# Kernel tuning notes

Hardware: AMD Instinct MI355X
Metric: run time of the kernel (lower is better)

Reference implementation:

```python
import jax, jax.numpy as jnp
import numpy as np

HID = 512      # hidden_size
IN = 1         # encoder/decoder input feature size
OUT = 1        # linear output size (feeds back as decoder input)
SEQ = 1000     # encoder sequence length
BATCH = 512
TGT = 1000     # target_len (decoder steps)


def setup_inputs() -> dict:
    key = jax.random.key(0)
    ks = jax.random.split(key, 11)
    s = 1.0 / np.sqrt(HID)  # PyTorch LSTM/Linear uniform init scale
    u = lambda k, shp: jax.random.uniform(k, shp, jnp.float32, -s, s)
    return {
        "input_batch": jax.random.normal(ks[0], (SEQ, BATCH, IN), jnp.float32),
        "enc_Wih": u(ks[1], (4 * HID, IN)),
        "enc_Whh": u(ks[2], (4 * HID, HID)),
        "enc_bih": u(ks[3], (4 * HID,)),
        "enc_bhh": u(ks[4], (4 * HID,)),
        "dec_Wih": u(ks[5], (4 * HID, OUT)),
        "dec_Whh": u(ks[6], (4 * HID, HID)),
        "dec_bih": u(ks[7], (4 * HID,)),
        "dec_bhh": u(ks[8], (4 * HID,)),
        "lin_W": u(ks[9], (OUT, HID)),
        "lin_b": u(ks[10], (OUT,)),
    }


def _lstm_cell(x, h, c, Wih, Whh, b):
    # PyTorch gate order: i, f, g, o
    gates = x @ Wih.T + h @ Whh.T + b  # [B, 4H]
    i, f, g, o = jnp.split(gates, 4, axis=-1)
    c = jax.nn.sigmoid(f) * c + jax.nn.sigmoid(i) * jnp.tanh(g)
    h = jax.nn.sigmoid(o) * jnp.tanh(c)
    return h, c


def reference(input_batch, enc_Wih, enc_Whh, enc_bih, enc_bhh,
              dec_Wih, dec_Whh, dec_bih, dec_bhh, lin_W, lin_b):
    batch = input_batch.shape[1]
    b_enc = enc_bih + enc_bhh
    b_dec = dec_bih + dec_bhh
    h0 = jnp.zeros((batch, HID), input_batch.dtype)

    # --- encoder: scan over SEQ time steps, zero initial state ---
    def enc_step(carry, x_t):
        h, c = carry
        h, c = _lstm_cell(x_t, h, c, enc_Wih, enc_Whh, b_enc)
        return (h, c), None

    (h, c), _ = jax.lax.scan(enc_step, (h0, h0), input_batch)

    x0 = jnp.zeros((batch, OUT), input_batch.dtype)

    def dec_step(carry, _):
        h, c, x = carry
        h, c = _lstm_cell(x, h, c, dec_Wih, dec_Whh, b_dec)
        pred = h @ lin_W.T + lin_b  # [B, OUT]
        return (h, c, pred), pred

    _, outputs = jax.lax.scan(dec_step, (h, c, x0), None, length=TGT)
    return outputs  # [TGT, BATCH, OUT]
```

## Files before the change

### kernel.cpp

```cpp
#include <hip/hip_runtime.h>


typedef _Float16 f16x8 __attribute__((ext_vector_type(8)));
typedef _Float16 f16x2 __attribute__((ext_vector_type(2)));
typedef float    f32x4 __attribute__((ext_vector_type(4)));
typedef unsigned long long u64;
typedef unsigned int u32;

#define GLOAD_LDS16(gp, lp)                                                    \
  __builtin_amdgcn_global_load_lds(                                            \
      (const __attribute__((address_space(1))) void*)(gp),                     \
      (__attribute__((address_space(3))) void*)(lp), 16, 0, 17)

__device__ __forceinline__ void store_h4_llc(_Float16* p, f16x2 v) {
  __hip_atomic_store((u32*)p, __builtin_bit_cast(u32, v),
                     __ATOMIC_RELAXED, __HIP_MEMORY_SCOPE_AGENT);
}

__device__ __forceinline__ float sigm(float x) {
  return __builtin_amdgcn_rcpf(1.0f + __expf(-x));
}
__device__ __forceinline__ float tanh_fast(float x) {
  float r = __expf(-2.0f*fabsf(x));
  float t = (1.0f - r)*__builtin_amdgcn_rcpf(1.0f + r);
  return copysignf(t, x);
}

__global__ void init_zero(float* __restrict__ out, int nout,
                          float* __restrict__ wsf, int nws) {
  int i = blockIdx.x*blockDim.x + threadIdx.x;
  int st = gridDim.x*blockDim.x;
  for (int j=i; j<nout; j+=st)
    __hip_atomic_store(&out[j], 0.f, __ATOMIC_RELAXED, __HIP_MEMORY_SCOPE_AGENT);
  for (int j=i; j<nws;  j+=st)
    __hip_atomic_store(&wsf[j], 0.f, __ATOMIC_RELAXED, __HIP_MEMORY_SCOPE_AGENT);
}

__global__ __launch_bounds__(256, 2) void lstm_main(
    const float* __restrict__ xin,
    const float* __restrict__ encWih, const float* __restrict__ encWhh,
    const float* __restrict__ enc_bih, const float* __restrict__ enc_bhh,
    const float* __restrict__ decWih, const float* __restrict__ decWhh,
    const float* __restrict__ dec_bih, const float* __restrict__ dec_bhh,
    const float* __restrict__ linW, const float* __restrict__ linb,
    float* __restrict__ out,
    _Float16* __restrict__ hbuf,
    int* __restrict__ flags)
{
  __shared__ f16x8 h_lds[2048];
  __shared__ float gates[32][68];

  const int bid = blockIdx.x, tid = threadIdx.x;
  const int rb = bid >> 5, hb = bid & 31;
  const int wid = tid >> 6, lane = tid & 63;
  const int lcol = lane & 15, lq = lane >> 4, kq = lq*8;

  const int b_local = tid >> 3, u0 = (tid & 7)*2;
  const int bg = rb*32 + b_local;
  const int jh0 = hb*16 + u0;

  float linw[2];
  #pragma unroll
  for (int u=0; u<2; ++u) linw[u] = linW[jh0+u];
  const float linbv = linb[0];

  f16x8 wHi[16], wLo[16];
  float biasv[8], wihv[8];
  float c[2] = {0.f, 0.f};
  int* myflag = flags + bid*32;
  const int* pollp = flags + (rb*32 + (lane & 31))*32;

  int goff[8];
  #pragma unroll
  for (int i=0; i<8; ++i) {
    const int cch = i*256 + tid;
    const int frag = cch >> 6;
    const int ks = frag >> 1, half = frag & 1;
    const int row_local = half*16 + (cch & 15);
    goff[i] = row_local*512 + ks*32 + ((cch >> 4) & 3)*8;
  }

  auto loadW = [&](const float* Whh, const float* bih, const float* bhh,
                   const float* Wih) {
    const int g = wid;
    const float* wr = Whh + (size_t)(g*512 + hb*16 + lcol)*512;
    #pragma unroll
    for (int ks=0; ks<16; ++ks) {
      f16x8 hi, lo;
      #pragma unroll
      for (int i=0; i<8; ++i) {
        float w = wr[ks*32 + kq + i];
        _Float16 hh = (_Float16)w;
        float hf = (float)hh;
        float rem = (w - hf)*2048.0f;
        if (fabsf(hf) < 6.104e-5f) { hh = (_Float16)0.0f; rem = w*2048.0f; }
        hi[i] = hh; lo[i] = (_Float16)rem;
      }
      wHi[ks] = hi; wLo[ks] = lo;
    }
    #pragma unroll
    for (int gg=0; gg<4; ++gg)
      #pragma unroll
      for (int u=0; u<2; ++u) {
        int j = gg*512 + jh0 + u;
        biasv[gg*2+u] = bih[j] + bhh[j];
        wihv[gg*2+u]  = Wih[j];
      }
  };

  loadW(encWhh, enc_bih, enc_bhh, encWih);

  for (int s=0; s<2000; ++s) {
    if (s == 1000) loadW(decWhh, dec_bih, dec_bhh, decWih);
    const bool dec = (s >= 1000);
    const int td = s - 1000;
    const _Float16* hr = hbuf + (size_t)((s+1)&1)*(512*512);
    _Float16*       hw = hbuf + (size_t)( s   &1)*(512*512);

    const _Float16* hrb = hr + (size_t)rb*32*512;
    f16x8* ldst = &h_lds[(size_t)wid*64];

    float x;
    if (!dec) x = xin[(size_t)s*512 + bg];
    else if (td == 0) x = 0.0f;
    else x = __hip_atomic_load(&out[(size_t)(td-1)*512 + bg],
                               __ATOMIC_RELAXED, __HIP_MEMORY_SCOPE_AGENT);

    #pragma unroll
    for (int i=0; i<8; ++i)
      GLOAD_LDS16(hrb + goff[i], ldst + i*256);
    __syncthreads();

    f32x4 accH[2], accL[2];
    accH[0] = {0.f,0.f,0.f,0.f}; accH[1] = {0.f,0.f,0.f,0.f};
    accL[0] = {0.f,0.f,0.f,0.f}; accL[1] = {0.f,0.f,0.f,0.f};

    #pragma unroll
    for (int ks=0; ks<16; ++ks) {
      const f16x8 a0 = h_lds[(ks*2+0)*64 + lane];
      const f16x8 a1 = h_lds[(ks*2+1)*64 + lane];
      accH[0] = __builtin_amdgcn_mfma_f32_16x16x32_f16(a0, wHi[ks], accH[0], 0,0,0);
      accH[1] = __builtin_amdgcn_mfma_f32_16x16x32_f16(a1, wHi[ks], accH[1], 0,0,0);
      accL[0] = __builtin_amdgcn_mfma_f32_16x16x32_f16(a0, wLo[ks], accL[0], 0,0,0);
      accL[1] = __builtin_amdgcn_mfma_f32_16x16x32_f16(a1, wLo[ks], accL[1], 0,0,0);
    }

    #pragma unroll
    for (int rt=0; rt<2; ++rt) {
      f32x4 v = accH[rt] + accL[rt]*(1.0f/2048.0f);
      const int col  = wid*16 + lcol;
      const int row0 = rt*16 + lq*4;
      #pragma unroll
      for (int i=0; i<4; ++i) gates[row0+i][col] = v[i];
    }
    __syncthreads();

    const float* grow = gates[b_local];
    f16x2 hv2;
    float sp = 0.f;
    #pragma unroll
    for (int u=0; u<2; ++u) {
      float ai = grow[ 0 + u0+u] + biasv[0+u] + x*wihv[0+u];
      float af = grow[16 + u0+u] + biasv[2+u] + x*wihv[2+u];
      float ag = grow[32 + u0+u] + biasv[4+u] + x*wihv[4+u];
      float ao = grow[48 + u0+u] + biasv[6+u] + x*wihv[6+u];
      float iv = sigm(ai);
      float fv = sigm(af);
      float gv = tanh_fast(ag);
      float ov = sigm(ao);
      float cn = fv*c[u] + iv*gv;
      c[u] = cn;
      float hv = ov*tanh_fast(cn);
      hv2[u] = (_Float16)hv;
      sp += hv*linw[u];
    }
    store_h4_llc(hw + (size_t)bg*512 + jh0, hv2);

    if (dec) {
      sp += __shfl_xor(sp, 1);
      sp += __shfl_xor(sp, 2);
      sp += __shfl_xor(sp, 4);
      if ((tid & 7) == 0) {
        float v = sp + (hb == 0 ? linbv : 0.f);
        __hip_atomic_fetch_add(&out[(size_t)td*512 + bg], v,
                               __ATOMIC_RELAXED, __HIP_MEMORY_SCOPE_AGENT);
      }
    }

    if (s != 1999) {
      asm volatile("s_waitcnt vmcnt(0)" ::: "memory");
      __syncthreads();
      const int av = s + 1;
      if (tid == 0)
        __hip_atomic_store(myflag, av, __ATOMIC_RELAXED, __HIP_MEMORY_SCOPE_AGENT);
      if (wid == 0) {
        while (!__all(__hip_atomic_load(pollp, __ATOMIC_RELAXED,
                                        __HIP_MEMORY_SCOPE_AGENT) >= av)) { }
      }
      __syncthreads();
    }
  }
}

extern "C" void kernel_launch(void* const* d_in, const int* in_sizes, int n_in,
                              void* d_out, int out_size, void* d_ws, size_t ws_size,
                              hipStream_t stream) {
  const float* xin     = (const float*)d_in[0];
  const float* encWih  = (const float*)d_in[1];
  const float* encWhh  = (const float*)d_in[2];
  const float* enc_bih = (const float*)d_in[3];
  const float* enc_bhh = (const float*)d_in[4];
  const float* decWih  = (const float*)d_in[5];
  const float* decWhh  = (const float*)d_in[6];
  const float* dec_bih = (const float*)d_in[7];
  const float* dec_bhh = (const float*)d_in[8];
  const float* linW    = (const float*)d_in[9];
  const float* linb    = (const float*)d_in[10];
  float* out = (float*)d_out;
  char* ws = (char*)d_ws;
  int* flags = (int*)ws;
  _Float16* hbuf = (_Float16*)(ws + 65536);

  init_zero<<<512, 256, 0, stream>>>(out, 1000*512, (float*)ws,
                                     (65536 + 2*512*512*2)/4);

  lstm_main<<<dim3(512), dim3(256), 0, stream>>>(
      xin, encWih, encWhh, enc_bih, enc_bhh,
      decWih, decWhh, dec_bih, dec_bhh,
      linW, linb, out, hbuf, flags);
}
```

Baseline: 12.53 ms.

## Split batch across twice as many blocks, 16 rows each

```diff
diff --git a/kernel.cpp b/kernel.cpp
--- a/kernel.cpp
+++ b/kernel.cpp
@@ -4,7 +4,6 @@
 typedef _Float16 f16x8 __attribute__((ext_vector_type(8)));
 typedef _Float16 f16x2 __attribute__((ext_vector_type(2)));
 typedef float    f32x4 __attribute__((ext_vector_type(4)));
-typedef unsigned long long u64;
 typedef unsigned int u32;
 
 #define GLOAD_LDS16(gp, lp)                                                    \
@@ -36,7 +35,7 @@
     __hip_atomic_store(&wsf[j], 0.f, __ATOMIC_RELAXED, __HIP_MEMORY_SCOPE_AGENT);
 }
 
-__global__ __launch_bounds__(256, 2) void lstm_main(
+__global__ __launch_bounds__(256, 4) void lstm_main(
     const float* __restrict__ xin,
     const float* __restrict__ encWih, const float* __restrict__ encWhh,
     const float* __restrict__ enc_bih, const float* __restrict__ enc_bhh,
@@ -47,16 +46,18 @@
     _Float16* __restrict__ hbuf,
     int* __restrict__ flags)
 {
-  __shared__ f16x8 h_lds[2048];
-  __shared__ float gates[32][68];
+  __shared__ f16x8 h_lds[1024];
+  __shared__ float gates[16][68];
 
   const int bid = blockIdx.x, tid = threadIdx.x;
   const int rb = bid >> 5, hb = bid & 31;
   const int wid = tid >> 6, lane = tid & 63;
   const int lcol = lane & 15, lq = lane >> 4, kq = lq*8;
 
-  const int b_local = tid >> 3, u0 = (tid & 7)*2;
-  const int bg = rb*32 + b_local;
+  const bool pw = (tid < 128);
+  const int b_local = tid >> 3;
+  const int u0 = (tid & 7)*2;
+  const int bg = rb*16 + (b_local & 15);
   const int jh0 = hb*16 + u0;
 
   float linw[2];
@@ -70,14 +71,12 @@
   int* myflag = flags + bid*32;
   const int* pollp = flags + (rb*32 + (lane & 31))*32;
 
-  int goff[8];
+  int goff[4];
   #pragma unroll
-  for (int i=0; i<8; ++i) {
+  for (int i=0; i<4; ++i) {
     const int cch = i*256 + tid;
-    const int frag = cch >> 6;
-    const int ks = frag >> 1, half = frag & 1;
-    const int row_local = half*16 + (cch & 15);
-    goff[i] = row_local*512 + ks*32 + ((cch >> 4) & 3)*8;
+    const int ks = cch >> 6, l = cch & 63;
+    goff[i] = (l & 15)*512 + ks*32 + (l >> 4)*8;
   }
 
   auto loadW = [&](const float* Whh, const float* bih, const float* bhh,
@@ -117,73 +116,70 @@
     const _Float16* hr = hbuf + (size_t)((s+1)&1)*(512*512);
     _Float16*       hw = hbuf + (size_t)( s   &1)*(512*512);
 
-    const _Float16* hrb = hr + (size_t)rb*32*512;
+    const _Float16* hrb = hr + (size_t)rb*16*512;
     f16x8* ldst = &h_lds[(size_t)wid*64];
 
-    float x;
-    if (!dec) x = xin[(size_t)s*512 + bg];
-    else if (td == 0) x = 0.0f;
-    else x = __hip_atomic_load(&out[(size_t)(td-1)*512 + bg],
-                               __ATOMIC_RELAXED, __HIP_MEMORY_SCOPE_AGENT);
-
-    #pragma unroll
-    for (int i=0; i<8; ++i)
+    float x = 0.0f;
+    if (pw) {
+      if (!dec) x = xin[(size_t)s*512 + bg];
+      else if (td > 0)
+        x = __hip_atomic_load(&out[(size_t)(td-1)*512 + bg],
+                              __ATOMIC_RELAXED, __HIP_MEMORY_SCOPE_AGENT);
+    }
+
+    #pragma unroll
+    for (int i=0; i<4; ++i)
       GLOAD_LDS16(hrb + goff[i], ldst + i*256);
     __syncthreads();
 
-    f32x4 accH[2], accL[2];
-    accH[0] = {0.f,0.f,0.f,0.f}; accH[1] = {0.f,0.f,0.f,0.f};
-    accL[0] = {0.f,0.f,0.f,0.f}; accL[1] = {0.f,0.f,0.f,0.f};
-
+    f32x4 accH = {0.f,0.f,0.f,0.f}, accL = {0.f,0.f,0.f,0.f};
     #pragma unroll
     for (int ks=0; ks<16; ++ks) {
-      const f16x8 a0 = h_lds[(ks*2+0)*64 + lane];
-      const f16x8 a1 = h_lds[(ks*2+1)*64 + lane];
-      accH[0] = __builtin_amdgcn_mfma_f32_16x16x32_f16(a0, wHi[ks], accH[0], 0,0,0);
-      accH[1] = __builtin_amdgcn_mfma_f32_16x16x32_f16(a1, wHi[ks], accH[1], 0,0,0);
-      accL[0] = __builtin_amdgcn_mfma_f32_16x16x32_f16(a0, wLo[ks], accL[0], 0,0,0);
-      accL[1] = __builtin_amdgcn_mfma_f32_16x16x32_f16(a1, wLo[ks], accL[1], 0,0,0);
-    }
-
-    #pragma unroll
-    for (int rt=0; rt<2; ++rt) {
-      f32x4 v = accH[rt] + accL[rt]*(1.0f/2048.0f);
+      const f16x8 a = h_lds[ks*64 + lane];
+      accH = __builtin_amdgcn_mfma_f32_16x16x32_f16(a, wHi[ks], accH, 0,0,0);
+      accL = __builtin_amdgcn_mfma_f32_16x16x32_f16(a, wLo[ks], accL, 0,0,0);
+    }
+
+    {
+      f32x4 v = accH + accL*(1.0f/2048.0f);
       const int col  = wid*16 + lcol;
-      const int row0 = rt*16 + lq*4;
+      const int row0 = lq*4;
       #pragma unroll
       for (int i=0; i<4; ++i) gates[row0+i][col] = v[i];
     }
     __syncthreads();
 
-    const float* grow = gates[b_local];
-    f16x2 hv2;
-    float sp = 0.f;
-    #pragma unroll
-    for (int u=0; u<2; ++u) {
-      float ai = grow[ 0 + u0+u] + biasv[0+u] + x*wihv[0+u];
-      float af = grow[16 + u0+u] + biasv[2+u] + x*wihv[2+u];
-      float ag = grow[32 + u0+u] + biasv[4+u] + x*wihv[4+u];
-      float ao = grow[48 + u0+u] + biasv[6+u] + x*wihv[6+u];
-      float iv = sigm(ai);
-      float fv = sigm(af);
-      float gv = tanh_fast(ag);
-      float ov = sigm(ao);
-      float cn = fv*c[u] + iv*gv;
-      c[u] = cn;
-      float hv = ov*tanh_fast(cn);
-      hv2[u] = (_Float16)hv;
-      sp += hv*linw[u];
-    }
-    store_h4_llc(hw + (size_t)bg*512 + jh0, hv2);
-
-    if (dec) {
-      sp += __shfl_xor(sp, 1);
-      sp += __shfl_xor(sp, 2);
-      sp += __shfl_xor(sp, 4);
-      if ((tid & 7) == 0) {
-        float v = sp + (hb == 0 ? linbv : 0.f);
-        __hip_atomic_fetch_add(&out[(size_t)td*512 + bg], v,
-                               __ATOMIC_RELAXED, __HIP_MEMORY_SCOPE_AGENT);
+    if (pw) {
+      const float* grow = gates[b_local & 15];
+      f16x2 hv2;
+      float sp = 0.f;
+      #pragma unroll
+      for (int u=0; u<2; ++u) {
+        float ai = grow[ 0 + u0+u] + biasv[0+u] + x*wihv[0+u];
+        float af = grow[16 + u0+u] + biasv[2+u] + x*wihv[2+u];
+        float ag = grow[32 + u0+u] + biasv[4+u] + x*wihv[4+u];
+        float ao = grow[48 + u0+u] + biasv[6+u] + x*wihv[6+u];
+        float iv = sigm(ai);
+        float fv = sigm(af);
+        float gv = tanh_fast(ag);
+        float ov = sigm(ao);
+        float cn = fv*c[u] + iv*gv;
+        c[u] = cn;
+        float hv = ov*tanh_fast(cn);
+        hv2[u] = (_Float16)hv;
+        sp += hv*linw[u];
+      }
+      store_h4_llc(hw + (size_t)bg*512 + jh0, hv2);
+
+      if (dec) {
+        sp += __shfl_xor(sp, 1);
+        sp += __shfl_xor(sp, 2);
+        sp += __shfl_xor(sp, 4);
+        if ((tid & 7) == 0) {
+          float v = sp + (hb == 0 ? linbv : 0.f);
+          __hip_atomic_fetch_add(&out[(size_t)td*512 + bg], v,
+                                 __ATOMIC_RELAXED, __HIP_MEMORY_SCOPE_AGENT);
+        }
       }
     }
 
@@ -219,12 +215,12 @@
   float* out = (float*)d_out;
   char* ws = (char*)d_ws;
   int* flags = (int*)ws;
-  _Float16* hbuf = (_Float16*)(ws + 65536);
+  _Float16* hbuf = (_Float16*)(ws + 131072);
 
   init_zero<<<512, 256, 0, stream>>>(out, 1000*512, (float*)ws,
-                                     (65536 + 2*512*512*2)/4);
-
-  lstm_main<<<dim3(512), dim3(256), 0, stream>>>(
+                                     (131072 + 2*512*512*2)/4);
+
+  lstm_main<<<dim3(1024), dim3(256), 0, stream>>>(
       xin, encWih, encWhh, enc_bih, enc_bhh,
       decWih, decWhh, dec_bih, dec_bhh,
       linW, linb, out, hbuf, flags);
```

New measurement: 25.43 ms. +102.9%, slower.

## Use per-wave flags and a partial-sum buffer to shorten the inter-block barrier

Applied to the files above, without the earlier changes.

```diff
diff --git a/kernel.cpp b/kernel.cpp
--- a/kernel.cpp
+++ b/kernel.cpp
@@ -4,6 +4,7 @@
 typedef _Float16 f16x8 __attribute__((ext_vector_type(8)));
 typedef _Float16 f16x2 __attribute__((ext_vector_type(2)));
 typedef float    f32x4 __attribute__((ext_vector_type(4)));
+typedef float    f32x2 __attribute__((ext_vector_type(2)));
 typedef unsigned long long u64;
 typedef unsigned int u32;
 
@@ -15,6 +16,11 @@
 __device__ __forceinline__ void store_h4_llc(_Float16* p, f16x2 v) {
   __hip_atomic_store((u32*)p, __builtin_bit_cast(u32, v),
                      __ATOMIC_RELAXED, __HIP_MEMORY_SCOPE_AGENT);
+}
+__device__ __forceinline__ f32x2 load_f2_llc(const float* p) {
+  u64 v = __hip_atomic_load((const u64*)p, __ATOMIC_RELAXED,
+                            __HIP_MEMORY_SCOPE_AGENT);
+  return __builtin_bit_cast(f32x2, v);
 }
 
 __device__ __forceinline__ float sigm(float x) {
@@ -45,7 +51,8 @@
     const float* __restrict__ linW, const float* __restrict__ linb,
     float* __restrict__ out,
     _Float16* __restrict__ hbuf,
-    int* __restrict__ flags)
+    int* __restrict__ flags,
+    float* __restrict__ part)
 {
   __shared__ f16x8 h_lds[2048];
   __shared__ float gates[32][68];
@@ -67,8 +74,9 @@
   f16x8 wHi[16], wLo[16];
   float biasv[8], wihv[8];
   float c[2] = {0.f, 0.f};
-  int* myflag = flags + bid*32;
-  const int* pollp = flags + (rb*32 + (lane & 31))*32;
+  int* myflag = flags + (bid*4 + wid)*32;
+  const int* p0 = flags + (rb*128 + lane)*32;
+  const int* p1 = flags + (rb*128 + 64 + lane)*32;
 
   int goff[8];
   #pragma unroll
@@ -120,11 +128,19 @@
     const _Float16* hrb = hr + (size_t)rb*32*512;
     f16x8* ldst = &h_lds[(size_t)wid*64];
 
-    float x;
-    if (!dec) x = xin[(size_t)s*512 + bg];
-    else if (td == 0) x = 0.0f;
-    else x = __hip_atomic_load(&out[(size_t)(td-1)*512 + bg],
-                               __ATOMIC_RELAXED, __HIP_MEMORY_SCOPE_AGENT);
+    float x = 0.0f;
+    if (!dec) {
+      x = xin[(size_t)s*512 + bg];
+    } else if (td > 0) {
+      const float* pb = part + (size_t)((td-1)&1)*16384 + bg*32 + (tid&7)*4;
+      f32x2 a = load_f2_llc(pb);
+      f32x2 b2 = load_f2_llc(pb + 2);
+      float sm = a[0] + a[1] + b2[0] + b2[1];
+      sm += __shfl_xor(sm, 1);
+      sm += __shfl_xor(sm, 2);
+      sm += __shfl_xor(sm, 4);
+      x = sm + linbv;
+    }
 
     #pragma unroll
     for (int i=0; i<8; ++i)
@@ -180,24 +196,36 @@
       sp += __shfl_xor(sp, 1);
       sp += __shfl_xor(sp, 2);
       sp += __shfl_xor(sp, 4);
-      if ((tid & 7) == 0) {
-        float v = sp + (hb == 0 ? linbv : 0.f);
-        __hip_atomic_fetch_add(&out[(size_t)td*512 + bg], v,
-                               __ATOMIC_RELAXED, __HIP_MEMORY_SCOPE_AGENT);
-      }
+      if ((tid & 7) == 0)
+        __hip_atomic_store(&part[(size_t)(td&1)*16384 + bg*32 + hb], sp,
+                           __ATOMIC_RELAXED, __HIP_MEMORY_SCOPE_AGENT);
     }
 
     if (s != 1999) {
       asm volatile("s_waitcnt vmcnt(0)" ::: "memory");
-      __syncthreads();
+      if (lane == 0)
+        __hip_atomic_store(myflag, s + 1, __ATOMIC_RELAXED,
+                           __HIP_MEMORY_SCOPE_AGENT);
+    }
+
+    if (dec && (tid & 7) == 0) {
+      float v = sp + (hb == 0 ? linbv : 0.f);
+      __hip_atomic_fetch_add(&out[(size_t)td*512 + bg], v,
+                             __ATOMIC_RELAXED, __HIP_MEMORY_SCOPE_AGENT);
+    }
+
+    if (s != 1999) {
       const int av = s + 1;
-      if (tid == 0)
-        __hip_atomic_store(myflag, av, __ATOMIC_RELAXED, __HIP_MEMORY_SCOPE_AGENT);
       if (wid == 0) {
-        while (!__all(__hip_atomic_load(pollp, __ATOMIC_RELAXED,
-                                        __HIP_MEMORY_SCOPE_AGENT) >= av)) { }
+        while (true) {
+          int f0 = __hip_atomic_load(p0, __ATOMIC_RELAXED, __HIP_MEMORY_SCOPE_AGENT);
+          int f1 = __hip_atomic_load(p1, __ATOMIC_RELAXED, __HIP_MEMORY_SCOPE_AGENT);
+          if (__all((f0 < av ? f0 : f1 < av ? f1 : av) >= av)) break;
+        }
       }
       __syncthreads();
+    } else {
+      asm volatile("s_waitcnt vmcnt(0)" ::: "memory");
     }
   }
 }
@@ -219,13 +247,14 @@
   float* out = (float*)d_out;
   char* ws = (char*)d_ws;
   int* flags = (int*)ws;
-  _Float16* hbuf = (_Float16*)(ws + 65536);
+  _Float16* hbuf = (_Float16*)(ws + 262144);
+  float* part = (float*)(ws + 262144 + 1048576);
 
   init_zero<<<512, 256, 0, stream>>>(out, 1000*512, (float*)ws,
-                                     (65536 + 2*512*512*2)/4);
+                                     (262144 + 1048576 + 131072)/4);
 
   lstm_main<<<dim3(512), dim3(256), 0, stream>>>(
       xin, encWih, encWhh, enc_bih, enc_bhh,
       decWih, decWhh, dec_bih, dec_bhh,
-      linW, linb, out, hbuf, flags);
-}
+      linW, linb, out, hbuf, flags, part);
+}
```

New measurement: 13.59 ms. +8.5%, slower.
